# Kernel optimization log

Hardware: AMD Instinct MI355X
Metric: run time of the kernel (lower is better)

The kernel has to match this reference:

```python
import jax, jax.numpy as jnp
import numpy as np

TOKENS = 512
IN_F = 8192
OUT_F = 8192
RANK = 64
NNZ = 8192
QMAX = 127.0  # int8 symmetric


def setup_inputs() -> dict:
    key = jax.random.key(0)
    ks = jax.random.split(key, 12)
    x = jax.random.normal(ks[0], (TOKENS, IN_F), dtype=jnp.float32)
    quantized_weight = jax.random.randint(ks[1], (OUT_F, IN_F), -128, 128, dtype=jnp.int32)
    weight_scale = jax.random.uniform(ks[2], (OUT_F,), minval=0.005, maxval=0.02, dtype=jnp.float32)
    smooth_scales = jax.random.uniform(ks[3], (IN_F,), minval=0.5, maxval=2.0, dtype=jnp.float32)
    act_scale = jnp.array([0.05], dtype=jnp.float32)
    outlier_rows = jax.random.randint(ks[4], (NNZ,), 0, OUT_F, dtype=jnp.int32)
    outlier_cols = jax.random.randint(ks[5], (NNZ,), 0, IN_F, dtype=jnp.int32)
    outlier_vals = jax.random.normal(ks[6], (NNZ,), dtype=jnp.float32) * 0.1
    svd_U = jax.random.normal(ks[7], (OUT_F, RANK), dtype=jnp.float32) * 0.02
    svd_S = jax.random.uniform(ks[8], (RANK,), minval=0.1, maxval=1.0, dtype=jnp.float32)
    svd_V = jax.random.normal(ks[9], (IN_F, RANK), dtype=jnp.float32) * 0.02
    bias = jax.random.normal(ks[10], (OUT_F,), dtype=jnp.float32) * 0.01
    return {"x": x, "quantized_weight": quantized_weight, "weight_scale": weight_scale,
            "smooth_scales": smooth_scales, "act_scale": act_scale,
            "outlier_rows": outlier_rows, "outlier_cols": outlier_cols,
            "outlier_vals": outlier_vals, "svd_U": svd_U, "svd_S": svd_S,
            "svd_V": svd_V, "bias": bias}


def reference(x, quantized_weight, weight_scale, smooth_scales, act_scale,
              outlier_rows, outlier_cols, outlier_vals, svd_U, svd_S, svd_V, bias):
    # SmoothQuant: migrate activation outliers into the weight scales
    x_s = x / smooth_scales  # [T, in]
    # per-tensor symmetric int8 activation fake-quant
    a = act_scale[0]
    x_q = jnp.clip(jnp.round(x_s / a), -QMAX - 1.0, QMAX)
    x_dq = x_q * a  # [T, in]
    # dequantize weight: per-output-channel scale, plus sparse outlier correction
    W = quantized_weight.astype(jnp.float32) * weight_scale[:, None]  # [out, in]
    W = W.at[outlier_rows, outlier_cols].add(outlier_vals)
    # dense quantized matmul
    y = x_dq @ W.T  # [T, out]
    # low-rank SVD residual: x @ (U S V^T)^T = ((x @ V) * S) @ U^T
    y = y + ((x_dq @ svd_V) * svd_S) @ svd_U.T
    return y + bias
```

## Files before the change

kernel.cpp:

```cpp
#include <hip/hip_runtime.h>
#include <hip/hip_bf16.h>

#define TOKENS 512
#define IN_F 8192
#define OUT_F 8192
#define RANK 64
#define NNZ 8192

#define KSPLIT 4
#define KRANGE (IN_F / KSPLIT)
#define BN 64
#define BK 64
#define NT (KRANGE / BK)

typedef __attribute__((ext_vector_type(8))) short short8;
typedef __attribute__((ext_vector_type(4))) float f32x4;
typedef __attribute__((ext_vector_type(4))) int int4v;

__device__ __forceinline__ unsigned short f2bf(float f) {
  unsigned int u = __builtin_bit_cast(unsigned int, f);
  u += 0x7FFFu + ((u >> 16) & 1u);
  return (unsigned short)(u >> 16);
}
__device__ __forceinline__ float bf2f(unsigned short b) {
  unsigned int u = ((unsigned int)b) << 16;
  return __builtin_bit_cast(float, u);
}

__device__ __forceinline__ void gload_lds16(const void* g, void* l) {
  __builtin_amdgcn_global_load_lds(
      (const __attribute__((address_space(1))) unsigned int*)(g),
      (__attribute__((address_space(3))) unsigned int*)(l), 16, 0, 0);
}

#define WAIT_VM(n) asm volatile("s_waitcnt vmcnt(" #n ")" ::: "memory")
#define WAIT_LGKM0 asm volatile("s_waitcnt lgkmcnt(0)" ::: "memory")

__global__ __launch_bounds__(256) void k_quant(const float* __restrict__ x,
                                               const float* __restrict__ smooth,
                                               const float* __restrict__ act,
                                               unsigned short* __restrict__ Abf,
                                               unsigned char* __restrict__ Aq) {
  int idx = blockIdx.x * 256 + threadIdx.x;
  int base = idx * 4;
  int col = base & (IN_F - 1);
  float a = act[0];
  float4 xx = *(const float4*)(x + base);
  float4 ss = *(const float4*)(smooth + col);
  float q0 = fminf(fmaxf(rintf((xx.x / ss.x) / a), -128.f), 127.f);
  float q1 = fminf(fmaxf(rintf((xx.y / ss.y) / a), -128.f), 127.f);
  float q2 = fminf(fmaxf(rintf((xx.z / ss.z) / a), -128.f), 127.f);
  float q3 = fminf(fmaxf(rintf((xx.w / ss.w) / a), -128.f), 127.f);
  ushort4 o;
  o.x = f2bf(q0); o.y = f2bf(q1); o.z = f2bf(q2); o.w = f2bf(q3);
  *(ushort4*)(Abf + base) = o;
  int i0 = (int)q0, i1 = (int)q1, i2 = (int)q2, i3 = (int)q3;
  unsigned int p = (i0 & 0xFF) | ((i1 & 0xFF) << 8) | ((i2 & 0xFF) << 16) |
                   ((unsigned)(i3 & 0xFF) << 24);
  *(unsigned int*)(Aq + base) = p;
}

__global__ __launch_bounds__(256) void k_lr1(const unsigned short* __restrict__ Abf,
                                             const float* __restrict__ V,
                                             const float* __restrict__ S,
                                             const float* __restrict__ act,
                                             float* __restrict__ t) {
  int bid = blockIdx.x;
  int mb = (bid & 3) * 128;
  int ksp = bid >> 2;
  int kb0 = ksp * KRANGE;
  int tid = threadIdx.x, w = tid >> 6, l = tid & 63;
  int lr = l & 15, lg = l >> 4;
  f32x4 acc[2][4] = {};
  for (int ks = 0; ks < KRANGE / 32; ++ks) {
    int kb = kb0 + ks * 32;
    short8 af[2];
#pragma unroll
    for (int fi = 0; fi < 2; ++fi) {
      int row = mb + w * 32 + fi * 16 + lr;
      af[fi] = *(const short8*)(Abf + (size_t)row * IN_F + kb + lg * 8);
    }
    short8 bfr[4];
#pragma unroll
    for (int fj = 0; fj < 4; ++fj) {
      int rk = fj * 16 + lr;
      short8 bv;
#pragma unroll
      for (int j = 0; j < 8; ++j)
        bv[j] = (short)f2bf(V[(size_t)(kb + lg * 8 + j) * RANK + rk]);
      bfr[fj] = bv;
    }
#pragma unroll
    for (int fi = 0; fi < 2; ++fi)
#pragma unroll
      for (int fj = 0; fj < 4; ++fj)
        acc[fi][fj] = __builtin_amdgcn_mfma_f32_16x16x32_bf16(af[fi], bfr[fj], acc[fi][fj], 0, 0, 0);
  }
  float a = act[0];
  float* tk = t + (size_t)ksp * TOKENS * RANK;
#pragma unroll
  for (int fi = 0; fi < 2; ++fi)
#pragma unroll
    for (int fj = 0; fj < 4; ++fj) {
      int rk = fj * 16 + lr;
      float sc = a * S[rk];
#pragma unroll
      for (int r = 0; r < 4; ++r) {
        int tok = mb + w * 32 + fi * 16 + lg * 4 + r;
        tk[(size_t)tok * RANK + rk] = acc[fi][fj][r] * sc;
      }
    }
}

__global__ __launch_bounds__(256) void k_lr2(const float* __restrict__ t,
                                             const float* __restrict__ U,
                                             const float* __restrict__ bias,
                                             float* __restrict__ out) {
  int bid = blockIdx.x;
  int mb = (bid & 3) * 128;
  int nb = (bid >> 2) * 128;
  int tid = threadIdx.x, w = tid >> 6, l = tid & 63;
  int lr = l & 15, lg = l >> 4;
  int wm = w >> 1, wn = w & 1;
  f32x4 acc[4][4] = {};
#pragma unroll
  for (int kk = 0; kk < 2; ++kk) {
    short8 af[4], bfr[4];
#pragma unroll
    for (int fi = 0; fi < 4; ++fi) {
      int row = mb + wm * 64 + fi * 16 + lr;
      size_t off = (size_t)row * RANK + kk * 32 + lg * 8;
      float4 t0 = {0, 0, 0, 0}, t1 = {0, 0, 0, 0};
#pragma unroll
      for (int s = 0; s < KSPLIT; ++s) {
        const float4* tp = (const float4*)(t + (size_t)s * TOKENS * RANK + off);
        float4 u0 = tp[0], u1 = tp[1];
        t0.x += u0.x; t0.y += u0.y; t0.z += u0.z; t0.w += u0.w;
        t1.x += u1.x; t1.y += u1.y; t1.z += u1.z; t1.w += u1.w;
      }
      af[fi][0] = f2bf(t0.x); af[fi][1] = f2bf(t0.y);
      af[fi][2] = f2bf(t0.z); af[fi][3] = f2bf(t0.w);
      af[fi][4] = f2bf(t1.x); af[fi][5] = f2bf(t1.y);
      af[fi][6] = f2bf(t1.z); af[fi][7] = f2bf(t1.w);
    }
#pragma unroll
    for (int fj = 0; fj < 4; ++fj) {
      int row = nb + wn * 64 + fj * 16 + lr;
      const float4* up = (const float4*)(U + (size_t)row * RANK + kk * 32 + lg * 8);
      float4 u0 = up[0], u1 = up[1];
      bfr[fj][0] = f2bf(u0.x); bfr[fj][1] = f2bf(u0.y);
      bfr[fj][2] = f2bf(u0.z); bfr[fj][3] = f2bf(u0.w);
      bfr[fj][4] = f2bf(u1.x); bfr[fj][5] = f2bf(u1.y);
      bfr[fj][6] = f2bf(u1.z); bfr[fj][7] = f2bf(u1.w);
    }
#pragma unroll
    for (int fi = 0; fi < 4; ++fi)
#pragma unroll
      for (int fj = 0; fj < 4; ++fj)
        acc[fi][fj] = __builtin_amdgcn_mfma_f32_16x16x32_bf16(af[fi], bfr[fj], acc[fi][fj], 0, 0, 0);
  }
#pragma unroll
  for (int fj = 0; fj < 4; ++fj) {
    int o = nb + wn * 64 + fj * 16 + lr;
    float b = bias[o];
#pragma unroll
    for (int fi = 0; fi < 4; ++fi)
#pragma unroll
      for (int r = 0; r < 4; ++r) {
        int tok = mb + wm * 64 + fi * 16 + lg * 4 + r;
        out[(size_t)tok * OUT_F + o] = b + acc[fi][fj][r];
      }
  }
}

__global__ __launch_bounds__(256) void k_outlier(const unsigned short* __restrict__ Abf,
                                                 const int* __restrict__ rows,
                                                 const int* __restrict__ cols,
                                                 const float* __restrict__ vals,
                                                 const float* __restrict__ act,
                                                 float* __restrict__ out) {
  __shared__ float accr[OUT_F];
  int tk = blockIdx.x;
  for (int i = threadIdx.x; i < OUT_F; i += 256) accr[i] = 0.f;
  __syncthreads();
  float a = act[0];
  for (int i = threadIdx.x; i < NNZ; i += 256) {
    int r = rows[i], c = cols[i];
    float v = vals[i];
    float xq = bf2f(Abf[(size_t)tk * IN_F + c]);
    atomicAdd(accr + r, a * xq * v);
  }
  __syncthreads();
  float* orow = out + (size_t)tk * OUT_F;
  for (int i = threadIdx.x; i < OUT_F; i += 256) orow[i] += accr[i];
}

__global__ __launch_bounds__(512, 4) void k_gemm(const unsigned char* __restrict__ Aq,
                                                 const int* __restrict__ W,
                                                 const float* __restrict__ wscale,
                                                 const float* __restrict__ act,
                                                 float* __restrict__ out) {
  __shared__ __align__(16) unsigned char As[2][512 * BK];
  __shared__ __align__(16) unsigned char Bs[2][BN * BK];

  int d = blockIdx.x;
  int xcd = d & 7, idx = d >> 3;
  int ks = xcd >> 1;
  int nb = idx * 2 + (xcd & 1);
  int kb0 = ks * KRANGE;

  int tid = threadIdx.x, w = tid >> 6, l = tid & 63;
  int lr = l & 15, lg = l >> 4;
  int wm = w >> 1, wn = w & 1;

  int4v acc[8][2] = {};
  int4v wa[2], wb[2];

  const int rB = tid >> 3;
  const int kcB = (tid & 7) * 8;

  auto LOAD_W = [&](int4v (&wr)[2], int kb) {
    const int* wp = W + (size_t)(nb * BN + rB) * IN_F + kb + kcB;
    wr[0] = *(const int4v*)wp;
    wr[1] = *(const int4v*)(wp + 4);
  };
  auto STAGE_A = [&](int buf, int kb) {
#pragma unroll
    for (int i = 0; i < 4; ++i) {
      int ubase = i * 512 + w * 64;
      int ell = ubase + l;
      int r = ell >> 2, up = ell & 3;
      int u = up ^ ((r >> 1) & 3);
      gload_lds16(Aq + (size_t)r * IN_F + kb + u * 16, &As[buf][(size_t)ubase * 16]);
    }
  };
  auto WRITE_B = [&](int buf, const int4v (&wr)[2]) {
    unsigned int w0 = 0, w1 = 0;
#pragma unroll
    for (int j = 0; j < 4; ++j) w0 |= ((unsigned)(wr[0][j] & 0xFF)) << (8 * j);
#pragma unroll
    for (int j = 0; j < 4; ++j) w1 |= ((unsigned)(wr[1][j] & 0xFF)) << (8 * j);
    int u = kcB >> 4, sub = (kcB >> 3) & 1;
    int us = u ^ ((rB >> 1) & 3);
    uint2 val; val.x = w0; val.y = w1;
    *(uint2*)(&Bs[buf][(size_t)rB * BK + us * 16 + sub * 8]) = val;
  };
  auto LDFA = [&](int buf, int row) -> int4v {
    int u = lg ^ ((row >> 1) & 3);
    return *(const int4v*)(&As[buf][(size_t)row * BK + u * 16]);
  };
  auto LDFB = [&](int buf, int row) -> int4v {
    int u = lg ^ ((row >> 1) & 3);
    return *(const int4v*)(&Bs[buf][(size_t)row * BK + u * 16]);
  };
  auto COMPUTE = [&](int buf) {
    __builtin_amdgcn_s_setprio(1);
    int4v b0 = LDFB(buf, wn * 32 + lr);
    int4v b1 = LDFB(buf, wn * 32 + 16 + lr);
#pragma unroll
    for (int fi = 0; fi < 8; ++fi) {
      int4v af = LDFA(buf, wm * 128 + fi * 16 + lr);
      acc[fi][0] = __builtin_amdgcn_mfma_i32_16x16x64_i8(af, b0, acc[fi][0], 0, 0, 0);
      acc[fi][1] = __builtin_amdgcn_mfma_i32_16x16x64_i8(af, b1, acc[fi][1], 0, 0, 0);
    }
    __builtin_amdgcn_s_setprio(0);
  };

  LOAD_W(wa, kb0);
  STAGE_A(0, kb0);
  WAIT_VM(4);
  WRITE_B(0, wa);
  LOAD_W(wa, kb0 + BK);
  WAIT_VM(2);
  WAIT_LGKM0;
  __builtin_amdgcn_s_barrier();

#define ITER(kt, CUR, wcur, wnxt)                                   \
  {                                                                 \
    STAGE_A(CUR ^ 1, kb0 + (((kt) + 1) & (NT - 1)) * BK);           \
    LOAD_W(wnxt, kb0 + (((kt) + 2) & (NT - 1)) * BK);               \
    COMPUTE(CUR);                                                   \
    WAIT_VM(6);                                                     \
    WRITE_B(CUR ^ 1, wcur);                                         \
    WAIT_VM(2);                                                     \
    WAIT_LGKM0;                                                     \
    __builtin_amdgcn_s_barrier();                                   \
  }

  for (int kt = 0; kt < NT; kt += 2) {
    ITER(kt, 0, wa, wb);
    ITER(kt + 1, 1, wb, wa);
  }
#undef ITER

  float a = act[0];
#pragma unroll
  for (int fj = 0; fj < 2; ++fj) {
    int o = nb * BN + wn * 32 + fj * 16 + lr;
    float sc = a * wscale[o];
#pragma unroll
    for (int fi = 0; fi < 8; ++fi)
#pragma unroll
      for (int rr = 0; rr < 4; ++rr) {
        int tok = wm * 128 + fi * 16 + lg * 4 + rr;
        atomicAdd(out + (size_t)tok * OUT_F + o, (float)acc[fi][fj][rr] * sc);
      }
  }
}

extern "C" void kernel_launch(void* const* d_in, const int* in_sizes, int n_in,
                              void* d_out, int out_size, void* d_ws, size_t ws_size,
                              hipStream_t stream) {
  const float* x = (const float*)d_in[0];
  const int* W = (const int*)d_in[1];
  const float* wscale = (const float*)d_in[2];
  const float* smooth = (const float*)d_in[3];
  const float* act = (const float*)d_in[4];
  const int* orow = (const int*)d_in[5];
  const int* ocol = (const int*)d_in[6];
  const float* oval = (const float*)d_in[7];
  const float* U = (const float*)d_in[8];
  const float* S = (const float*)d_in[9];
  const float* V = (const float*)d_in[10];
  const float* bias = (const float*)d_in[11];
  float* out = (float*)d_out;

  unsigned short* Abf = (unsigned short*)d_ws;
  unsigned char* Aq = (unsigned char*)d_ws + (size_t)TOKENS * IN_F * 2;
  float* t = (float*)((char*)d_ws + (size_t)TOKENS * IN_F * 3);

  k_quant<<<(TOKENS * IN_F / 4) / 256, 256, 0, stream>>>(x, smooth, act, Abf, Aq);
  k_lr1<<<16, 256, 0, stream>>>(Abf, V, S, act, t);
  k_lr2<<<256, 256, 0, stream>>>(t, U, bias, out);
  k_outlier<<<TOKENS, 256, 0, stream>>>(Abf, orow, ocol, oval, act, out);
  k_gemm<<<512, 512, 0, stream>>>(Aq, W, wscale, act, out);
}
```

Measured before the change: 217.2 us.

## Drop split-K in int8 GEMM, tile M instead; atomic-accumulate low-rank partials

The main int8 GEMM no longer splits K four ways with atomic adds. Each block now covers a 256-token by 64-output tile over the full K, so the epilogue does a plain read-add-write on the output. Previously every block staged all 512 token rows of A with K split four ways. Now A is split across two M tiles, so the W tile is loaded twice but A staging per block is halved and there are no float atomics in the output. The low-rank first stage now uses 64 blocks that atomically add into a zeroed buffer, replacing four partial buffers that the second stage had to sum. Running with fewer GEMM blocks (256) and a lower occupancy hint may leave parallelism unused.

```diff
diff --git a/kernel.cpp b/kernel.cpp
--- a/kernel.cpp
+++ b/kernel.cpp
@@ -7,11 +7,10 @@
 #define RANK 64
 #define NNZ 8192
 
-#define KSPLIT 4
-#define KRANGE (IN_F / KSPLIT)
+#define BM 256
 #define BN 64
 #define BK 64
-#define NT (KRANGE / BK)
+#define NT (IN_F / BK)
 
 typedef __attribute__((ext_vector_type(8))) short short8;
 typedef __attribute__((ext_vector_type(4))) float f32x4;
@@ -67,12 +66,11 @@
                                              float* __restrict__ t) {
   int bid = blockIdx.x;
   int mb = (bid & 3) * 128;
-  int ksp = bid >> 2;
-  int kb0 = ksp * KRANGE;
+  int kb0 = (bid >> 2) * 512;
   int tid = threadIdx.x, w = tid >> 6, l = tid & 63;
   int lr = l & 15, lg = l >> 4;
   f32x4 acc[2][4] = {};
-  for (int ks = 0; ks < KRANGE / 32; ++ks) {
+  for (int ks = 0; ks < 16; ++ks) {
     int kb = kb0 + ks * 32;
     short8 af[2];
 #pragma unroll
@@ -97,7 +95,6 @@
         acc[fi][fj] = __builtin_amdgcn_mfma_f32_16x16x32_bf16(af[fi], bfr[fj], acc[fi][fj], 0, 0, 0);
   }
   float a = act[0];
-  float* tk = t + (size_t)ksp * TOKENS * RANK;
 #pragma unroll
   for (int fi = 0; fi < 2; ++fi)
 #pragma unroll
@@ -107,7 +104,7 @@
 #pragma unroll
       for (int r = 0; r < 4; ++r) {
         int tok = mb + w * 32 + fi * 16 + lg * 4 + r;
-        tk[(size_t)tok * RANK + rk] = acc[fi][fj][r] * sc;
+        atomicAdd(t + tok * RANK + rk, acc[fi][fj][r] * sc);
       }
     }
 }
@@ -129,15 +126,8 @@
 #pragma unroll
     for (int fi = 0; fi < 4; ++fi) {
       int row = mb + wm * 64 + fi * 16 + lr;
-      size_t off = (size_t)row * RANK + kk * 32 + lg * 8;
-      float4 t0 = {0, 0, 0, 0}, t1 = {0, 0, 0, 0};
-#pragma unroll
-      for (int s = 0; s < KSPLIT; ++s) {
-        const float4* tp = (const float4*)(t + (size_t)s * TOKENS * RANK + off);
-        float4 u0 = tp[0], u1 = tp[1];
-        t0.x += u0.x; t0.y += u0.y; t0.z += u0.z; t0.w += u0.w;
-        t1.x += u1.x; t1.y += u1.y; t1.z += u1.z; t1.w += u1.w;
-      }
+      const float4* tp = (const float4*)(t + (size_t)row * RANK + kk * 32 + lg * 8);
+      float4 t0 = tp[0], t1 = tp[1];
       af[fi][0] = f2bf(t0.x); af[fi][1] = f2bf(t0.y);
       af[fi][2] = f2bf(t0.z); af[fi][3] = f2bf(t0.w);
       af[fi][4] = f2bf(t1.x); af[fi][5] = f2bf(t1.y);
@@ -195,25 +185,24 @@
   for (int i = threadIdx.x; i < OUT_F; i += 256) orow[i] += accr[i];
 }
 
-__global__ __launch_bounds__(512, 4) void k_gemm(const unsigned char* __restrict__ Aq,
+__global__ __launch_bounds__(512, 2) void k_gemm(const unsigned char* __restrict__ Aq,
                                                  const int* __restrict__ W,
                                                  const float* __restrict__ wscale,
                                                  const float* __restrict__ act,
                                                  float* __restrict__ out) {
-  __shared__ __align__(16) unsigned char As[2][512 * BK];
+  __shared__ __align__(16) unsigned char As[2][BM * BK];
   __shared__ __align__(16) unsigned char Bs[2][BN * BK];
 
   int d = blockIdx.x;
-  int xcd = d & 7, idx = d >> 3;
-  int ks = xcd >> 1;
-  int nb = idx * 2 + (xcd & 1);
-  int kb0 = ks * KRANGE;
+  int wg = (d & 7) * 32 + (d >> 3);
+  int mb = wg >> 7;
+  int nb = wg & 127;
 
   int tid = threadIdx.x, w = tid >> 6, l = tid & 63;
   int lr = l & 15, lg = l >> 4;
   int wm = w >> 1, wn = w & 1;
 
-  int4v acc[8][2] = {};
+  int4v acc[4][2] = {};
   int4v wa[2], wb[2];
 
   const int rB = tid >> 3;
@@ -226,12 +215,13 @@
   };
   auto STAGE_A = [&](int buf, int kb) {
 #pragma unroll
-    for (int i = 0; i < 4; ++i) {
+    for (int i = 0; i < 2; ++i) {
       int ubase = i * 512 + w * 64;
       int ell = ubase + l;
       int r = ell >> 2, up = ell & 3;
       int u = up ^ ((r >> 1) & 3);
-      gload_lds16(Aq + (size_t)r * IN_F + kb + u * 16, &As[buf][(size_t)ubase * 16]);
+      gload_lds16(Aq + (size_t)(mb * BM + r) * IN_F + kb + u * 16,
+                  &As[buf][(size_t)ubase * 16]);
     }
   };
   auto WRITE_B = [&](int buf, const int4v (&wr)[2]) {
@@ -258,29 +248,29 @@
     int4v b0 = LDFB(buf, wn * 32 + lr);
     int4v b1 = LDFB(buf, wn * 32 + 16 + lr);
 #pragma unroll
-    for (int fi = 0; fi < 8; ++fi) {
-      int4v af = LDFA(buf, wm * 128 + fi * 16 + lr);
+    for (int fi = 0; fi < 4; ++fi) {
+      int4v af = LDFA(buf, wm * 64 + fi * 16 + lr);
       acc[fi][0] = __builtin_amdgcn_mfma_i32_16x16x64_i8(af, b0, acc[fi][0], 0, 0, 0);
       acc[fi][1] = __builtin_amdgcn_mfma_i32_16x16x64_i8(af, b1, acc[fi][1], 0, 0, 0);
     }
     __builtin_amdgcn_s_setprio(0);
   };
 
-  LOAD_W(wa, kb0);
-  STAGE_A(0, kb0);
-  WAIT_VM(4);
+  LOAD_W(wa, 0);
+  STAGE_A(0, 0);
+  WAIT_VM(2);
   WRITE_B(0, wa);
-  LOAD_W(wa, kb0 + BK);
+  LOAD_W(wa, BK);
   WAIT_VM(2);
   WAIT_LGKM0;
   __builtin_amdgcn_s_barrier();
 
 #define ITER(kt, CUR, wcur, wnxt)                                   \
   {                                                                 \
-    STAGE_A(CUR ^ 1, kb0 + (((kt) + 1) & (NT - 1)) * BK);           \
-    LOAD_W(wnxt, kb0 + (((kt) + 2) & (NT - 1)) * BK);               \
+    STAGE_A(CUR ^ 1, (((kt) + 1) & (NT - 1)) * BK);                 \
+    LOAD_W(wnxt, (((kt) + 2) & (NT - 1)) * BK);                     \
     COMPUTE(CUR);                                                   \
-    WAIT_VM(6);                                                     \
+    WAIT_VM(4);                                                     \
     WRITE_B(CUR ^ 1, wcur);                                         \
     WAIT_VM(2);                                                     \
     WAIT_LGKM0;                                                     \
@@ -299,11 +289,12 @@
     int o = nb * BN + wn * 32 + fj * 16 + lr;
     float sc = a * wscale[o];
 #pragma unroll
-    for (int fi = 0; fi < 8; ++fi)
+    for (int fi = 0; fi < 4; ++fi)
 #pragma unroll
       for (int rr = 0; rr < 4; ++rr) {
-        int tok = wm * 128 + fi * 16 + lg * 4 + rr;
-        atomicAdd(out + (size_t)tok * OUT_F + o, (float)acc[fi][fj][rr] * sc);
+        int tok = mb * BM + wm * 64 + fi * 16 + lg * 4 + rr;
+        float* p = out + (size_t)tok * OUT_F + o;
+        *p += (float)acc[fi][fj][rr] * sc;
       }
   }
 }
@@ -329,9 +320,10 @@
   unsigned char* Aq = (unsigned char*)d_ws + (size_t)TOKENS * IN_F * 2;
   float* t = (float*)((char*)d_ws + (size_t)TOKENS * IN_F * 3);
 
+  hipMemsetAsync(t, 0, TOKENS * RANK * sizeof(float), stream);
   k_quant<<<(TOKENS * IN_F / 4) / 256, 256, 0, stream>>>(x, smooth, act, Abf, Aq);
-  k_lr1<<<16, 256, 0, stream>>>(Abf, V, S, act, t);
+  k_lr1<<<64, 256, 0, stream>>>(Abf, V, S, act, t);
   k_lr2<<<256, 256, 0, stream>>>(t, U, bias, out);
   k_outlier<<<TOKENS, 256, 0, stream>>>(Abf, orow, ocol, oval, act, out);
-  k_gemm<<<512, 512, 0, stream>>>(Aq, W, wscale, act, out);
-}
+  k_gemm<<<256, 512, 0, stream>>>(Aq, W, wscale, act, out);
+}
```

Result: faster. 204.1 us (-6.0%).

## Replace split-K atomics with int partial buffers merged in outlier kernel

Applied to the files above, without the earlier changes.

The int8 GEMM now writes raw int32 split-K partials to a workspace buffer instead of doing float atomicAdd into the output. A new merge kernel sums the four partials, applies the activation and weight scales, and adds the outlier contributions in one pass. The low-rank first stage now uses 64 blocks with atomic accumulation into a zeroed buffer rather than a 4-way partial array. The block-to-XCD mapping in the GEMM is also changed. This removes output atomics, but it adds 32 MB of partial writes and reads plus a memset.

```diff
diff --git a/kernel.cpp b/kernel.cpp
--- a/kernel.cpp
+++ b/kernel.cpp
@@ -9,6 +9,7 @@
 
 #define KSPLIT 4
 #define KRANGE (IN_F / KSPLIT)
+#define BM 512
 #define BN 64
 #define BK 64
 #define NT (KRANGE / BK)
@@ -67,12 +68,11 @@
                                              float* __restrict__ t) {
   int bid = blockIdx.x;
   int mb = (bid & 3) * 128;
-  int ksp = bid >> 2;
-  int kb0 = ksp * KRANGE;
+  int kb0 = (bid >> 2) * 512;
   int tid = threadIdx.x, w = tid >> 6, l = tid & 63;
   int lr = l & 15, lg = l >> 4;
   f32x4 acc[2][4] = {};
-  for (int ks = 0; ks < KRANGE / 32; ++ks) {
+  for (int ks = 0; ks < 16; ++ks) {
     int kb = kb0 + ks * 32;
     short8 af[2];
 #pragma unroll
@@ -97,7 +97,6 @@
         acc[fi][fj] = __builtin_amdgcn_mfma_f32_16x16x32_bf16(af[fi], bfr[fj], acc[fi][fj], 0, 0, 0);
   }
   float a = act[0];
-  float* tk = t + (size_t)ksp * TOKENS * RANK;
 #pragma unroll
   for (int fi = 0; fi < 2; ++fi)
 #pragma unroll
@@ -107,7 +106,7 @@
 #pragma unroll
       for (int r = 0; r < 4; ++r) {
         int tok = mb + w * 32 + fi * 16 + lg * 4 + r;
-        tk[(size_t)tok * RANK + rk] = acc[fi][fj][r] * sc;
+        atomicAdd(t + tok * RANK + rk, acc[fi][fj][r] * sc);
       }
     }
 }
@@ -129,15 +128,8 @@
 #pragma unroll
     for (int fi = 0; fi < 4; ++fi) {
       int row = mb + wm * 64 + fi * 16 + lr;
-      size_t off = (size_t)row * RANK + kk * 32 + lg * 8;
-      float4 t0 = {0, 0, 0, 0}, t1 = {0, 0, 0, 0};
-#pragma unroll
-      for (int s = 0; s < KSPLIT; ++s) {
-        const float4* tp = (const float4*)(t + (size_t)s * TOKENS * RANK + off);
-        float4 u0 = tp[0], u1 = tp[1];
-        t0.x += u0.x; t0.y += u0.y; t0.z += u0.z; t0.w += u0.w;
-        t1.x += u1.x; t1.y += u1.y; t1.z += u1.z; t1.w += u1.w;
-      }
+      const float4* tp = (const float4*)(t + (size_t)row * RANK + kk * 32 + lg * 8);
+      float4 t0 = tp[0], t1 = tp[1];
       af[fi][0] = f2bf(t0.x); af[fi][1] = f2bf(t0.y);
       af[fi][2] = f2bf(t0.z); af[fi][3] = f2bf(t0.w);
       af[fi][4] = f2bf(t1.x); af[fi][5] = f2bf(t1.y);
@@ -173,12 +165,11 @@
   }
 }
 
-__global__ __launch_bounds__(256) void k_outlier(const unsigned short* __restrict__ Abf,
-                                                 const int* __restrict__ rows,
-                                                 const int* __restrict__ cols,
-                                                 const float* __restrict__ vals,
-                                                 const float* __restrict__ act,
-                                                 float* __restrict__ out) {
+__global__ __launch_bounds__(256) void k_outlier_merge(
+    const unsigned short* __restrict__ Abf, const int* __restrict__ rows,
+    const int* __restrict__ cols, const float* __restrict__ vals,
+    const float* __restrict__ act, const float* __restrict__ wscale,
+    const int* __restrict__ part, float* __restrict__ out) {
   __shared__ float accr[OUT_F];
   int tk = blockIdx.x;
   for (int i = threadIdx.x; i < OUT_F; i += 256) accr[i] = 0.f;
@@ -192,21 +183,35 @@
   }
   __syncthreads();
   float* orow = out + (size_t)tk * OUT_F;
-  for (int i = threadIdx.x; i < OUT_F; i += 256) orow[i] += accr[i];
+  const int* p0 = part + (size_t)tk * OUT_F;
+  const int* p1 = p0 + (size_t)TOKENS * OUT_F;
+  const int* p2 = p1 + (size_t)TOKENS * OUT_F;
+  const int* p3 = p2 + (size_t)TOKENS * OUT_F;
+  for (int i = threadIdx.x * 4; i < OUT_F; i += 1024) {
+    int4v s0 = *(const int4v*)(p0 + i);
+    int4v s1 = *(const int4v*)(p1 + i);
+    int4v s2 = *(const int4v*)(p2 + i);
+    int4v s3 = *(const int4v*)(p3 + i);
+    float4 ws = *(const float4*)(wscale + i);
+    float4 ov = *(const float4*)(orow + i);
+    ov.x += accr[i + 0] + (float)(s0[0] + s1[0] + s2[0] + s3[0]) * a * ws.x;
+    ov.y += accr[i + 1] + (float)(s0[1] + s1[1] + s2[1] + s3[1]) * a * ws.y;
+    ov.z += accr[i + 2] + (float)(s0[2] + s1[2] + s2[2] + s3[2]) * a * ws.z;
+    ov.w += accr[i + 3] + (float)(s0[3] + s1[3] + s2[3] + s3[3]) * a * ws.w;
+    *(float4*)(orow + i) = ov;
+  }
 }
 
 __global__ __launch_bounds__(512, 4) void k_gemm(const unsigned char* __restrict__ Aq,
                                                  const int* __restrict__ W,
-                                                 const float* __restrict__ wscale,
-                                                 const float* __restrict__ act,
-                                                 float* __restrict__ out) {
-  __shared__ __align__(16) unsigned char As[2][512 * BK];
+                                                 int* __restrict__ part) {
+  __shared__ __align__(16) unsigned char As[2][BM * BK];
   __shared__ __align__(16) unsigned char Bs[2][BN * BK];
 
   int d = blockIdx.x;
-  int xcd = d & 7, idx = d >> 3;
-  int ks = xcd >> 1;
-  int nb = idx * 2 + (xcd & 1);
+  int wg = (d & 7) * 64 + (d >> 3);
+  int ks = wg >> 7;
+  int nb = wg & 127;
   int kb0 = ks * KRANGE;
 
   int tid = threadIdx.x, w = tid >> 6, l = tid & 63;
@@ -293,17 +298,16 @@
   }
 #undef ITER
 
-  float a = act[0];
+  int* pp = part + (size_t)ks * TOKENS * OUT_F;
 #pragma unroll
   for (int fj = 0; fj < 2; ++fj) {
     int o = nb * BN + wn * 32 + fj * 16 + lr;
-    float sc = a * wscale[o];
 #pragma unroll
     for (int fi = 0; fi < 8; ++fi)
 #pragma unroll
       for (int rr = 0; rr < 4; ++rr) {
         int tok = wm * 128 + fi * 16 + lg * 4 + rr;
-        atomicAdd(out + (size_t)tok * OUT_F + o, (float)acc[fi][fj][rr] * sc);
+        pp[(size_t)tok * OUT_F + o] = acc[fi][fj][rr];
       }
   }
 }
@@ -328,10 +332,13 @@
   unsigned short* Abf = (unsigned short*)d_ws;
   unsigned char* Aq = (unsigned char*)d_ws + (size_t)TOKENS * IN_F * 2;
   float* t = (float*)((char*)d_ws + (size_t)TOKENS * IN_F * 3);
-
+  int* part = (int*)((char*)d_ws + (size_t)TOKENS * IN_F * 3 + (size_t)TOKENS * RANK * 4);
+
+  hipMemsetAsync(t, 0, TOKENS * RANK * sizeof(float), stream);
   k_quant<<<(TOKENS * IN_F / 4) / 256, 256, 0, stream>>>(x, smooth, act, Abf, Aq);
-  k_lr1<<<16, 256, 0, stream>>>(Abf, V, S, act, t);
+  k_gemm<<<512, 512, 0, stream>>>(Aq, W, part);
+  k_lr1<<<64, 256, 0, stream>>>(Abf, V, S, act, t);
   k_lr2<<<256, 256, 0, stream>>>(t, U, bias, out);
-  k_outlier<<<TOKENS, 256, 0, stream>>>(Abf, orow, ocol, oval, act, out);
-  k_gemm<<<512, 512, 0, stream>>>(Aq, W, wscale, act, out);
-}
+  k_outlier_merge<<<TOKENS, 256, 0, stream>>>(Abf, orow, ocol, oval, act,
+                                              wscale, part, out);
+}
```

After: 191.1 us. 1.14x faster.
